# Kernel optimization log

Measured on AMD Instinct MI355X. Metric: run time of the kernel, lower is better.

## Reference

```python
import jax, jax.numpy as jnp
import numpy as np

B, S, D_MODEL, HEAD = 4, 4096, 1024, 64


def rope(x):
    # Faithful to the torch code: 'odd' = even-indexed elems, 'even' = odd-indexed.
    b, s, d = x.shape
    half = d // 2
    pos = jnp.arange(s, dtype=x.dtype)
    theta = 1.0 / (10000.0 ** (jnp.arange(half, dtype=x.dtype) / half))
    freqs = pos[:, None] * theta[None, :]  # (s, half)
    sin, cos = jnp.sin(freqs), jnp.cos(freqs)
    odd = x[..., 0::2]
    even = x[..., 1::2]
    x_rot_even = even * cos + odd * sin
    x_rot_odd = odd * cos - even * sin
    return jnp.stack([x_rot_odd, x_rot_even], axis=-1).reshape(x.shape)


def setup_inputs() -> dict:
    key = jax.random.key(0)
    kx, kq, kk, kv = jax.random.split(key, 4)
    x = jax.random.normal(kx, (B, S, D_MODEL), dtype=jnp.float32)
    # torch Linear weights are [out,in]; we store the transposed [in,out] form.
    sc = 1.0 / np.sqrt(D_MODEL)
    Wq = jax.random.normal(kq, (D_MODEL, HEAD), dtype=jnp.float32) * sc
    Wk = jax.random.normal(kk, (D_MODEL, HEAD), dtype=jnp.float32) * sc
    Wv = jax.random.normal(kv, (D_MODEL, HEAD), dtype=jnp.float32) * sc
    return {"x": x, "Wq": Wq, "Wk": Wk, "Wv": Wv}


def reference(x, Wq, Wk, Wv):
    Q = rope(x @ Wq)  # (B, S, H)
    K = rope(x @ Wk)
    V = x @ Wv
    scale = K.shape[-1] ** -0.5
    scores = jnp.einsum('bqh,bkh->bqk', Q, K) * scale  # (B, S, S)
    causal = jnp.tril(jnp.ones((S, S), dtype=bool))
    scores = jnp.where(causal, scores, -jnp.inf)
    probs = jax.nn.softmax(scores, axis=-1)  # dropout p treated as 0 (eval)
    return jnp.einsum('bqk,bkh->bqh', probs, V)
```

## Files before the change

### kernel.cpp

```cpp
#include <hip/hip_runtime.h>
#include <stdint.h>


static constexpr int S_LEN  = 4096;
static constexpr int DMODEL = 1024;
static constexpr int NS     = 6;
static constexpr float SHIFT = 8.0f;

typedef __attribute__((ext_vector_type(8))) short bf16x8;
typedef __attribute__((ext_vector_type(4))) float f32x4;

#define MFMA16(a, b, c) __builtin_amdgcn_mfma_f32_16x16x32_bf16((a), (b), (c), 0, 0, 0)

__device__ __forceinline__ unsigned short f2b(float f) {
    union { float f; unsigned int u; } v;
    v.f = f;
    unsigned int u = v.u;
    u += 0x7fffu + ((u >> 16) & 1u);
    return (unsigned short)(u >> 16);
}
__device__ __forceinline__ float b2f(unsigned short b) {
    union { unsigned int u; float f; } v;
    v.u = ((unsigned int)b) << 16;
    return v.f;
}

template <int CTRL>
__device__ __forceinline__ float dpp_f(float v) {
    return __builtin_bit_cast(float,
        __builtin_amdgcn_update_dpp(0, __builtin_bit_cast(int, v), CTRL, 0xf, 0xf, false));
}
__device__ __forceinline__ float rowsum16(float v) {
    v += dpp_f<0x128>(v);
    v += dpp_f<0x124>(v);
    v += dpp_f<0x122>(v);
    v += dpp_f<0x121>(v);
    return v;
}

__device__ __forceinline__ void dma16(const void* g, void* l) {
    __builtin_amdgcn_global_load_lds(
        (const __attribute__((address_space(1))) unsigned int*)g,
        (__attribute__((address_space(3))) unsigned int*)l, 16, 0, 0);
}

__global__ __launch_bounds__(256) void prep_wt(const float* __restrict__ Wq,
                                               const float* __restrict__ Wk,
                                               const float* __restrict__ Wv,
                                               unsigned short* __restrict__ Wt) {
    int idx = blockIdx.x * 256 + threadIdx.x;
    int c = idx >> 10;
    int k = idx & 1023;
    int mat = c >> 6, n = c & 63;
    const float* W = (mat == 0) ? Wq : (mat == 1) ? Wk : Wv;
    Wt[idx] = f2b(W[k * 64 + n]);
}

__global__ __launch_bounds__(256) void proj_rope(const float* __restrict__ x,
                                                 const unsigned short* __restrict__ Wt,
                                                 unsigned short* __restrict__ Qg,
                                                 unsigned short* __restrict__ Kg,
                                                 unsigned short* __restrict__ Vtg) {
    __shared__ __align__(16) float          Xs[2][64 * 64];
    __shared__ __align__(16) unsigned short Bs[2][192 * 64];

    const int tid  = threadIdx.x;
    const int wave = tid >> 6, lane = tid & 63;
    const int l15  = lane & 15, quad = lane >> 4;
    const int rbase = blockIdx.x * 64;

    f32x4 acc[4][3];
#pragma unroll
    for (int mf = 0; mf < 4; ++mf)
#pragma unroll
        for (int ft = 0; ft < 3; ++ft) acc[mf][ft] = (f32x4){0.f, 0.f, 0.f, 0.f};

    const float* xg = x + (size_t)rbase * DMODEL;

    auto stage = [&](int kc, int buf) {
#pragma unroll
        for (int ii = 0; ii < 4; ++ii) {
            const int i = 4 * wave + ii;
            const int row = i * 4 + (lane >> 4);
            const int gd = lane & 15;
            const int gs = (gd & 8) | ((gd & 7) ^ (row & 7));
            dma16(xg + (size_t)row * DMODEL + kc * 64 + gs * 4, &Xs[buf][i * 256]);
        }
#pragma unroll
        for (int jj = 0; jj < 6; ++jj) {
            const int j = 6 * wave + jj;
            const int col = j * 8 + (lane >> 3);
            const int gd = lane & 7;
            const int gs = gd ^ (col & 7);
            dma16(Wt + (size_t)col * 1024 + kc * 64 + gs * 8, &Bs[buf][j * 512]);
        }
    };

    stage(0, 0);
    int p = 0;
    const int msk = l15 & 7;

#pragma unroll 1
    for (int kc = 0; kc < 16; ++kc) {
        __syncthreads();
        if (kc + 1 < 16) stage(kc + 1, p ^ 1);

        const float* Xb = &Xs[p][0];
        const unsigned short* Bb = &Bs[p][0];

#pragma unroll
        for (int kk2 = 0; kk2 < 2; ++kk2) {
            bf16x8 bf0 = *reinterpret_cast<const bf16x8*>(
                Bb + (wave * 48 + 0 * 16 + l15) * 64 + ((kk2 * 4 + quad) ^ msk) * 8);
            bf16x8 bf1 = *reinterpret_cast<const bf16x8*>(
                Bb + (wave * 48 + 1 * 16 + l15) * 64 + ((kk2 * 4 + quad) ^ msk) * 8);
            bf16x8 bf2 = *reinterpret_cast<const bf16x8*>(
                Bb + (wave * 48 + 2 * 16 + l15) * 64 + ((kk2 * 4 + quad) ^ msk) * 8);
#pragma unroll
            for (int mf = 0; mf < 4; ++mf) {
                const int row = mf * 16 + l15;
                float4 a0 = *reinterpret_cast<const float4*>(
                    Xb + row * 64 + (kk2 * 8 + ((quad * 2) ^ msk)) * 4);
                float4 a1 = *reinterpret_cast<const float4*>(
                    Xb + row * 64 + (kk2 * 8 + ((quad * 2 + 1) ^ msk)) * 4);
                bf16x8 af;
                af[0] = (short)f2b(a0.x); af[1] = (short)f2b(a0.y);
                af[2] = (short)f2b(a0.z); af[3] = (short)f2b(a0.w);
                af[4] = (short)f2b(a1.x); af[5] = (short)f2b(a1.y);
                af[6] = (short)f2b(a1.z); af[7] = (short)f2b(a1.w);
                acc[mf][0] = MFMA16(af, bf0, acc[mf][0]);
                acc[mf][1] = MFMA16(af, bf1, acc[mf][1]);
                acc[mf][2] = MFMA16(af, bf2, acc[mf][2]);
            }
        }
        p ^= 1;
    }

#pragma unroll
    for (int ft = 0; ft < 3; ++ft) {
        const int col0 = wave * 48 + ft * 16;
        const int mat  = col0 >> 6;
        const int d    = (col0 & 63) + l15;
        float theta = 0.f;
        if (mat < 2) {
            int i = d >> 1;
            theta = exp2f((float)i * -0.41524101186f);
        }
#pragma unroll
        for (int mf = 0; mf < 4; ++mf) {
#pragma unroll
            for (int r = 0; r < 4; ++r) {
                const int gr   = rbase + mf * 16 + quad * 4 + r;
                const int b    = gr >> 12;
                const int spos = gr & (S_LEN - 1);
                float v = acc[mf][ft][r];
                if (mat < 2) {
                    float partner = __shfl_xor(v, 1);
                    float fr = (float)spos * theta;
                    float sn = __sinf(fr);
                    float cs = __cosf(fr);
                    float outv = (d & 1) ? (v * cs + partner * sn)
                                         : (v * cs - partner * sn);
                    if (mat == 0) outv *= 0.125f;
                    unsigned short bv = f2b(outv);
                    if (mat == 0) Qg[(size_t)gr * 64 + d] = bv;
                    else          Kg[(size_t)gr * 64 + d] = bv;
                } else {
                    Vtg[(size_t)b * (64 * S_LEN) + (size_t)d * S_LEN + spos] = f2b(v);
                }
            }
        }
    }
}

__global__ __launch_bounds__(256) void attn_split(const unsigned short* __restrict__ Qg,
                                                  const unsigned short* __restrict__ Kg,
                                                  const unsigned short* __restrict__ Vtg,
                                                  unsigned short* __restrict__ OP,
                                                  float* __restrict__ L) {
    __shared__ __align__(16) unsigned short Klds[2][64 * 64];
    __shared__ __align__(16) unsigned short Vlds[2][64 * 64];
    __shared__ __align__(16) unsigned short Plds[4][16 * 72];

    const int tid  = threadIdx.x;
    const int wave = tid >> 6, lane = tid & 63;
    const int l15  = lane & 15, quad = lane >> 4;
    const int qt = 63 - blockIdx.x;
    const int split = blockIdx.y, b = blockIdx.z;
    const int qbase = qt * 64;

    const int total = qt + 1;
    const int chunk = (total + NS - 1) / NS;
    const int k0 = split * chunk;
    const int k1 = (k0 + chunk < total) ? (k0 + chunk) : total;

    bf16x8 qa[2];
    {
        const unsigned short* qrow = Qg + (size_t)(b * S_LEN + qbase + wave * 16 + l15) * 64;
        qa[0] = *reinterpret_cast<const bf16x8*>(qrow + quad * 8);
        qa[1] = *reinterpret_cast<const bf16x8*>(qrow + 32 + quad * 8);
    }

    f32x4 o[4];
    float lsum[4];
#pragma unroll
    for (int nt = 0; nt < 4; ++nt) o[nt] = (f32x4){0.f, 0.f, 0.f, 0.f};
#pragma unroll
    for (int r = 0; r < 4; ++r) lsum[r] = 0.f;

    const unsigned short* kgb = Kg  + (size_t)(b * S_LEN) * 64;
    const unsigned short* vgb = Vtg + (size_t)b * (64 * S_LEN);
    unsigned short* Pw = &Plds[wave][0];

    const int i0 = 2 * wave, i1 = 2 * wave + 1;
    const int r0 = (i0 * 64 + lane) >> 3, g0 = (i0 * 64 + lane) & 7;
    const int r1 = (i1 * 64 + lane) >> 3, g1 = (i1 * 64 + lane) & 7;
    const int sg0 = (g0 ^ (r0 & 7)) * 8, sg1 = (g1 ^ (r1 & 7)) * 8;

    auto stage = [&](int kt, int buf) {
        const unsigned short* kp = kgb + (size_t)kt * 64 * 64;
        dma16(kp + r0 * 64 + sg0, &Klds[buf][i0 * 512]);
        dma16(kp + r1 * 64 + sg1, &Klds[buf][i1 * 512]);
        const unsigned short* vp = vgb + (size_t)kt * 64;
        dma16(vp + (size_t)r0 * S_LEN + sg0, &Vlds[buf][i0 * 512]);
        dma16(vp + (size_t)r1 * S_LEN + sg1, &Vlds[buf][i1 * 512]);
    };

    if (k0 < k1) stage(k0, 0);

    int p = 0;
    for (int kt = k0; kt < k1; ++kt) {
        __syncthreads();
        if (kt + 1 < k1) stage(kt + 1, p ^ 1);

        const unsigned short* Kb = &Klds[p][0];
        const unsigned short* Vb = &Vlds[p][0];

        f32x4 s[4];
#pragma unroll
        for (int nt = 0; nt < 4; ++nt) {
            const int rk = nt * 16 + l15;
            bf16x8 kb0 = *reinterpret_cast<const bf16x8*>(Kb + rk * 64 + ((quad ^ (rk & 7)) * 8));
            bf16x8 kb1 = *reinterpret_cast<const bf16x8*>(Kb + rk * 64 + (((4 + quad) ^ (rk & 7)) * 8));
            f32x4 z = (f32x4){0.f, 0.f, 0.f, 0.f};
            z = MFMA16(qa[0], kb0, z);
            z = MFMA16(qa[1], kb1, z);
            s[nt] = z;
        }

        if (kt == qt) {
#pragma unroll
            for (int nt = 0; nt < 4; ++nt) {
                int key_l = nt * 16 + l15;
#pragma unroll
                for (int r = 0; r < 4; ++r) {
                    int q_l = wave * 16 + quad * 4 + r;
                    if (key_l > q_l) s[nt][r] = -1e30f;
                }
            }
        }

#pragma unroll
        for (int nt = 0; nt < 4; ++nt)
#pragma unroll
            for (int r = 0; r < 4; ++r) {
                float pv = __expf(s[nt][r] - SHIFT);
                s[nt][r] = pv;
                lsum[r] += pv;
            }

#pragma unroll
        for (int nt = 0; nt < 4; ++nt)
#pragma unroll
            for (int r = 0; r < 4; ++r)
                Pw[(quad * 4 + r) * 72 + nt * 16 + l15] = f2b(s[nt][r]);

#pragma unroll
        for (int kc = 0; kc < 2; ++kc) {
            bf16x8 pa = *reinterpret_cast<const bf16x8*>(Pw + l15 * 72 + kc * 32 + quad * 8);
#pragma unroll
            for (int nt = 0; nt < 4; ++nt) {
                const int rv = nt * 16 + l15;
                bf16x8 vb = *reinterpret_cast<const bf16x8*>(
                    Vb + rv * 64 + (((kc * 4 + quad) ^ (rv & 7)) * 8));
                o[nt] = MFMA16(pa, vb, o[nt]);
            }
        }
        p ^= 1;
    }

#pragma unroll
    for (int r = 0; r < 4; ++r) lsum[r] = rowsum16(lsum[r]);

    const size_t prow_base = ((size_t)(split * 4 + b)) * S_LEN;
#pragma unroll
    for (int nt = 0; nt < 4; ++nt)
#pragma unroll
        for (int r = 0; r < 4; ++r) {
            int row = qbase + wave * 16 + quad * 4 + r;
            OP[(prow_base + row) * 64 + nt * 16 + l15] = f2b(o[nt][r]);
        }
    if (l15 == 0) {
#pragma unroll
        for (int r = 0; r < 4; ++r) {
            int row = qbase + wave * 16 + quad * 4 + r;
            L[prow_base + row] = lsum[r];
        }
    }
}

__global__ __launch_bounds__(256) void combine(const unsigned short* __restrict__ OP,
                                               const float* __restrict__ L,
                                               float* __restrict__ out) {
    int idx = blockIdx.x * 256 + threadIdx.x;
    int d   = idx & 63;
    int row = (idx >> 6) & (S_LEN - 1);
    int b   = idx >> 18;

    float num = 0.f, den = 0.f;
#pragma unroll
    for (int s = 0; s < NS; ++s) {
        size_t pr = (size_t)(s * 4 + b) * S_LEN + row;
        den += L[pr];
        num += b2f(OP[pr * 64 + d]);
    }
    out[idx] = num / den;
}

extern "C" void kernel_launch(void* const* d_in, const int* in_sizes, int n_in,
                              void* d_out, int out_size, void* d_ws, size_t ws_size,
                              hipStream_t stream) {
    const float* x  = (const float*)d_in[0];
    const float* Wq = (const float*)d_in[1];
    const float* Wk = (const float*)d_in[2];
    const float* Wv = (const float*)d_in[3];
    float* out = (float*)d_out;

    unsigned char* base = (unsigned char*)d_ws;
    unsigned short* Qg  = (unsigned short*)(base);
    unsigned short* Kg  = (unsigned short*)(base + (2u << 20));
    unsigned short* Vtg = (unsigned short*)(base + (4u << 20));
    unsigned short* Wt  = (unsigned short*)(base + (6u << 20));
    float*          L   = (float*)(base + (6u << 20) + (1u << 19));
    unsigned short* OP  = (unsigned short*)(base + (7u << 20));

    prep_wt<<<768, 256, 0, stream>>>(Wq, Wk, Wv, Wt);
    proj_rope<<<256, 256, 0, stream>>>(x, Wt, Qg, Kg, Vtg);
    attn_split<<<dim3(64, NS, 4), 256, 0, stream>>>(Qg, Kg, Vtg, OP, L);
    combine<<<4096, 256, 0, stream>>>(OP, L, out);
}
```

Before: 161.1 us.

## Split projection output columns across two blocks and remap waves to rows

```diff
diff --git a/kernel.cpp b/kernel.cpp
--- a/kernel.cpp
+++ b/kernel.cpp
@@ -56,26 +56,26 @@
     Wt[idx] = f2b(W[k * 64 + n]);
 }
 
-__global__ __launch_bounds__(256) void proj_rope(const float* __restrict__ x,
-                                                 const unsigned short* __restrict__ Wt,
-                                                 unsigned short* __restrict__ Qg,
-                                                 unsigned short* __restrict__ Kg,
-                                                 unsigned short* __restrict__ Vtg) {
+__global__ __launch_bounds__(256, 2) void proj_rope(const float* __restrict__ x,
+                                                    const unsigned short* __restrict__ Wt,
+                                                    unsigned short* __restrict__ Qg,
+                                                    unsigned short* __restrict__ Kg,
+                                                    unsigned short* __restrict__ Vtg) {
     __shared__ __align__(16) float          Xs[2][64 * 64];
-    __shared__ __align__(16) unsigned short Bs[2][192 * 64];
+    __shared__ __align__(16) unsigned short Bs[2][96 * 64];
 
     const int tid  = threadIdx.x;
     const int wave = tid >> 6, lane = tid & 63;
     const int l15  = lane & 15, quad = lane >> 4;
-    const int rbase = blockIdx.x * 64;
-
-    f32x4 acc[4][3];
-#pragma unroll
-    for (int mf = 0; mf < 4; ++mf)
-#pragma unroll
-        for (int ft = 0; ft < 3; ++ft) acc[mf][ft] = (f32x4){0.f, 0.f, 0.f, 0.f};
+    const int rbase = (blockIdx.x >> 1) * 64;
+    const int ch    = blockIdx.x & 1;
+
+    f32x4 acc[6];
+#pragma unroll
+    for (int ft = 0; ft < 6; ++ft) acc[ft] = (f32x4){0.f, 0.f, 0.f, 0.f};
 
     const float* xg = x + (size_t)rbase * DMODEL;
+    const unsigned short* wg = Wt + (size_t)(ch * 96) * 1024;
 
     auto stage = [&](int kc, int buf) {
 #pragma unroll
@@ -87,12 +87,12 @@
             dma16(xg + (size_t)row * DMODEL + kc * 64 + gs * 4, &Xs[buf][i * 256]);
         }
 #pragma unroll
-        for (int jj = 0; jj < 6; ++jj) {
-            const int j = 6 * wave + jj;
+        for (int jj = 0; jj < 3; ++jj) {
+            const int j = 3 * wave + jj;
             const int col = j * 8 + (lane >> 3);
             const int gd = lane & 7;
             const int gs = gd ^ (col & 7);
-            dma16(Wt + (size_t)col * 1024 + kc * 64 + gs * 8, &Bs[buf][j * 512]);
+            dma16(wg + (size_t)col * 1024 + kc * 64 + gs * 8, &Bs[buf][j * 512]);
         }
     };
 
@@ -107,38 +107,32 @@
 
         const float* Xb = &Xs[p][0];
         const unsigned short* Bb = &Bs[p][0];
+        const int arow = wave * 16 + l15;
 
 #pragma unroll
         for (int kk2 = 0; kk2 < 2; ++kk2) {
-            bf16x8 bf0 = *reinterpret_cast<const bf16x8*>(
-                Bb + (wave * 48 + 0 * 16 + l15) * 64 + ((kk2 * 4 + quad) ^ msk) * 8);
-            bf16x8 bf1 = *reinterpret_cast<const bf16x8*>(
-                Bb + (wave * 48 + 1 * 16 + l15) * 64 + ((kk2 * 4 + quad) ^ msk) * 8);
-            bf16x8 bf2 = *reinterpret_cast<const bf16x8*>(
-                Bb + (wave * 48 + 2 * 16 + l15) * 64 + ((kk2 * 4 + quad) ^ msk) * 8);
-#pragma unroll
-            for (int mf = 0; mf < 4; ++mf) {
-                const int row = mf * 16 + l15;
-                float4 a0 = *reinterpret_cast<const float4*>(
-                    Xb + row * 64 + (kk2 * 8 + ((quad * 2) ^ msk)) * 4);
-                float4 a1 = *reinterpret_cast<const float4*>(
-                    Xb + row * 64 + (kk2 * 8 + ((quad * 2 + 1) ^ msk)) * 4);
-                bf16x8 af;
-                af[0] = (short)f2b(a0.x); af[1] = (short)f2b(a0.y);
-                af[2] = (short)f2b(a0.z); af[3] = (short)f2b(a0.w);
-                af[4] = (short)f2b(a1.x); af[5] = (short)f2b(a1.y);
-                af[6] = (short)f2b(a1.z); af[7] = (short)f2b(a1.w);
-                acc[mf][0] = MFMA16(af, bf0, acc[mf][0]);
-                acc[mf][1] = MFMA16(af, bf1, acc[mf][1]);
-                acc[mf][2] = MFMA16(af, bf2, acc[mf][2]);
+            float4 a0 = *reinterpret_cast<const float4*>(
+                Xb + arow * 64 + (kk2 * 8 + ((quad * 2) ^ msk)) * 4);
+            float4 a1 = *reinterpret_cast<const float4*>(
+                Xb + arow * 64 + (kk2 * 8 + ((quad * 2 + 1) ^ msk)) * 4);
+            bf16x8 af;
+            af[0] = (short)f2b(a0.x); af[1] = (short)f2b(a0.y);
+            af[2] = (short)f2b(a0.z); af[3] = (short)f2b(a0.w);
+            af[4] = (short)f2b(a1.x); af[5] = (short)f2b(a1.y);
+            af[6] = (short)f2b(a1.z); af[7] = (short)f2b(a1.w);
+#pragma unroll
+            for (int ft = 0; ft < 6; ++ft) {
+                bf16x8 bf = *reinterpret_cast<const bf16x8*>(
+                    Bb + (ft * 16 + l15) * 64 + ((kk2 * 4 + quad) ^ msk) * 8);
+                acc[ft] = MFMA16(af, bf, acc[ft]);
             }
         }
         p ^= 1;
     }
 
 #pragma unroll
-    for (int ft = 0; ft < 3; ++ft) {
-        const int col0 = wave * 48 + ft * 16;
+    for (int ft = 0; ft < 6; ++ft) {
+        const int col0 = ch * 96 + ft * 16;
         const int mat  = col0 >> 6;
         const int d    = (col0 & 63) + l15;
         float theta = 0.f;
@@ -147,27 +141,24 @@
             theta = exp2f((float)i * -0.41524101186f);
         }
 #pragma unroll
-        for (int mf = 0; mf < 4; ++mf) {
-#pragma unroll
-            for (int r = 0; r < 4; ++r) {
-                const int gr   = rbase + mf * 16 + quad * 4 + r;
-                const int b    = gr >> 12;
-                const int spos = gr & (S_LEN - 1);
-                float v = acc[mf][ft][r];
-                if (mat < 2) {
-                    float partner = __shfl_xor(v, 1);
-                    float fr = (float)spos * theta;
-                    float sn = __sinf(fr);
-                    float cs = __cosf(fr);
-                    float outv = (d & 1) ? (v * cs + partner * sn)
-                                         : (v * cs - partner * sn);
-                    if (mat == 0) outv *= 0.125f;
-                    unsigned short bv = f2b(outv);
-                    if (mat == 0) Qg[(size_t)gr * 64 + d] = bv;
-                    else          Kg[(size_t)gr * 64 + d] = bv;
-                } else {
-                    Vtg[(size_t)b * (64 * S_LEN) + (size_t)d * S_LEN + spos] = f2b(v);
-                }
+        for (int r = 0; r < 4; ++r) {
+            const int gr   = rbase + wave * 16 + quad * 4 + r;
+            const int b    = gr >> 12;
+            const int spos = gr & (S_LEN - 1);
+            float v = acc[ft][r];
+            if (mat < 2) {
+                float partner = __shfl_xor(v, 1);
+                float fr = (float)spos * theta;
+                float sn = __sinf(fr);
+                float cs = __cosf(fr);
+                float outv = (d & 1) ? (v * cs + partner * sn)
+                                     : (v * cs - partner * sn);
+                if (mat == 0) outv *= 0.125f;
+                unsigned short bv = f2b(outv);
+                if (mat == 0) Qg[(size_t)gr * 64 + d] = bv;
+                else          Kg[(size_t)gr * 64 + d] = bv;
+            } else {
+                Vtg[(size_t)b * (64 * S_LEN) + (size_t)d * S_LEN + spos] = f2b(v);
             }
         }
     }
@@ -345,7 +336,7 @@
     unsigned short* OP  = (unsigned short*)(base + (7u << 20));
 
     prep_wt<<<768, 256, 0, stream>>>(Wq, Wk, Wv, Wt);
-    proj_rope<<<256, 256, 0, stream>>>(x, Wt, Qg, Kg, Vtg);
+    proj_rope<<<512, 256, 0, stream>>>(x, Wt, Qg, Kg, Vtg);
     attn_split<<<dim3(64, NS, 4), 256, 0, stream>>>(Qg, Kg, Vtg, OP, L);
     combine<<<4096, 256, 0, stream>>>(OP, L, out);
 }
```

Measured after the change: 156.5 us. -2.9%, faster.
